# Kernel optimization log

Measured on AMD Instinct MI355X. Metric: run time of the kernel, lower is better.

The kernel has to match this reference:

```python
import jax, jax.numpy as jnp
import numpy as np

NUM_TOKENS = 8192
TWO_D = 22016  # 2 * intermediate_size (LLaMA-7B: d = 11008)
DEQUANT_SCALE = 0.0008


def setup_inputs() -> dict:
    key = jax.random.key(0)
    # int32 accumulators from an int8 gate_up GEMM: symmetric around 0
    x = jax.random.randint(key, (NUM_TOKENS, TWO_D), -128, 128, dtype=jnp.int32)
    dequant_scale = jnp.float32(DEQUANT_SCALE)
    return {"x": x, "dequant_scale": dequant_scale}


def reference(x, dequant_scale):
    # Dequant -> SiLU(gate) * up -> per-token abs-max int8 requant.
    d = x.shape[1] // 2
    xf = x.astype(jnp.float32) * dequant_scale          # dequantize
    gate = xf[:, :d]
    up = xf[:, d:]
    tmp = jax.nn.silu(gate) * up                        # (num_tokens, d) fp32
    # per-token quant scale = absmax / 127
    scale = jnp.max(jnp.abs(tmp), axis=1) / jnp.float32(127.0)  # (num_tokens,)
    q = jnp.clip(jnp.round(tmp / scale[:, None]), -128.0, 127.0).astype(jnp.int8)
    return (q, scale)
```

## Files before the change

### kernel.cpp

```cpp
#include <hip/hip_runtime.h>


constexpr int NUM_TOKENS = 8192;
constexpr int TWO_D      = 22016;
constexpr int D          = TWO_D / 2;
constexpr int VEC        = D / 4;
constexpr int THREADS    = 512;
constexpr int NWAVES     = THREADS / 64;
constexpr int FULL_ITERS = VEC / THREADS;
constexpr int REM        = VEC % THREADS;

typedef int   i32x4 __attribute__((ext_vector_type(4)));
typedef float f32x4 __attribute__((ext_vector_type(4)));

__device__ __forceinline__ float silu_mul(float g, float u) {
    return g * __builtin_amdgcn_rcpf(1.0f + __expf(-g)) * u;
}

__global__ __launch_bounds__(THREADS)
void dsmq_kernel(const i32x4* __restrict__ x,
                 const float* __restrict__ dsp,
                 f32x4* __restrict__ qout,
                 float* __restrict__ sout)
{
    const int row = blockIdx.x;
    const int t   = threadIdx.x;
    const float ds = *dsp;

    const i32x4* gp = x + (size_t)row * (TWO_D / 4);
    const i32x4* up = gp + VEC;

    f32x4 tmp[FULL_ITERS + 1];
    float m = 0.0f;

#pragma unroll
    for (int k = 0; k <= FULL_ITERS; ++k) {
        const int idx = k * THREADS + t;
        if (k < FULL_ITERS || t < REM) {
            const i32x4 gv = __builtin_nontemporal_load(&gp[idx]);
            const i32x4 uv = __builtin_nontemporal_load(&up[idx]);
            f32x4 r;
            r.x = silu_mul((float)gv.x * ds, (float)uv.x * ds);
            r.y = silu_mul((float)gv.y * ds, (float)uv.y * ds);
            r.z = silu_mul((float)gv.z * ds, (float)uv.z * ds);
            r.w = silu_mul((float)gv.w * ds, (float)uv.w * ds);
            tmp[k] = r;
            m = fmaxf(m, fmaxf(fmaxf(fabsf(r.x), fabsf(r.y)),
                               fmaxf(fabsf(r.z), fabsf(r.w))));
        }
    }

#pragma unroll
    for (int off = 32; off >= 1; off >>= 1)
        m = fmaxf(m, __shfl_xor(m, off, 64));

    __shared__ float smax[NWAVES];
    const int wave = t >> 6;
    if ((t & 63) == 0) smax[wave] = m;
    __syncthreads();
    m = smax[0];
#pragma unroll
    for (int w = 1; w < NWAVES; ++w) m = fmaxf(m, smax[w]);

    const float scale = m / 127.0f;
    const float inv   = (m > 0.0f) ? 127.0f / m : 0.0f;

    if (t == 0) sout[row] = scale;

    f32x4* qp = qout + (size_t)row * VEC;
#pragma unroll
    for (int k = 0; k <= FULL_ITERS; ++k) {
        const int idx = k * THREADS + t;
        if (k < FULL_ITERS || t < REM) {
            const f32x4 r = tmp[k];
            f32x4 q;
            q.x = fminf(fmaxf(rintf(r.x * inv), -128.0f), 127.0f);
            q.y = fminf(fmaxf(rintf(r.y * inv), -128.0f), 127.0f);
            q.z = fminf(fmaxf(rintf(r.z * inv), -128.0f), 127.0f);
            q.w = fminf(fmaxf(rintf(r.w * inv), -128.0f), 127.0f);
            __builtin_nontemporal_store(q, &qp[idx]);
        }
    }
}

extern "C" void kernel_launch(void* const* d_in, const int* in_sizes, int n_in,
                              void* d_out, int out_size, void* d_ws, size_t ws_size,
                              hipStream_t stream)
{
    const i32x4* x  = (const i32x4*)d_in[0];
    const float* ds = (const float*)d_in[1];
    f32x4* qout = (f32x4*)d_out;
    float* sout = (float*)d_out + (size_t)NUM_TOKENS * D;
    dsmq_kernel<<<NUM_TOKENS, THREADS, 0, stream>>>(x, ds, qout, sout);
}
```

Baseline: 181.0 us.

## Process two rows per block, overlapping row1 loads with row0 quantized stores

Each block now handles two tokens. The second row's loads and SiLU compute are interleaved with the quantize-and-store pass of the first row, so memory reads and writes overlap within a block instead of running in separate phases. The grid is halved, which cuts per-block launch and reduction overhead but gives fewer blocks to schedule. Register pressure stays similar because the tmp array is reused across the two rows.

```diff
diff --git a/kernel.cpp b/kernel.cpp
--- a/kernel.cpp
+++ b/kernel.cpp
@@ -7,6 +7,7 @@
 constexpr int VEC        = D / 4;
 constexpr int THREADS    = 512;
 constexpr int NWAVES     = THREADS / 64;
+constexpr int ITERS      = (VEC + THREADS - 1) / THREADS;
 constexpr int FULL_ITERS = VEC / THREADS;
 constexpr int REM        = VEC % THREADS;
 
@@ -17,68 +18,95 @@
     return g * __builtin_amdgcn_rcpf(1.0f + __expf(-g)) * u;
 }
 
+__device__ __forceinline__ f32x4 silu4(const i32x4 gv, const i32x4 uv, float ds, float& m) {
+    f32x4 r;
+    r.x = silu_mul((float)gv.x * ds, (float)uv.x * ds);
+    r.y = silu_mul((float)gv.y * ds, (float)uv.y * ds);
+    r.z = silu_mul((float)gv.z * ds, (float)uv.z * ds);
+    r.w = silu_mul((float)gv.w * ds, (float)uv.w * ds);
+    m = fmaxf(m, fmaxf(fmaxf(fabsf(r.x), fabsf(r.y)),
+                       fmaxf(fabsf(r.z), fabsf(r.w))));
+    return r;
+}
+
+__device__ __forceinline__ f32x4 quant4(const f32x4 r, float inv) {
+    f32x4 q;
+    q.x = fminf(fmaxf(rintf(r.x * inv), -128.0f), 127.0f);
+    q.y = fminf(fmaxf(rintf(r.y * inv), -128.0f), 127.0f);
+    q.z = fminf(fmaxf(rintf(r.z * inv), -128.0f), 127.0f);
+    q.w = fminf(fmaxf(rintf(r.w * inv), -128.0f), 127.0f);
+    return q;
+}
+
+__device__ __forceinline__ float block_max(float m, volatile float* smax, int t) {
+#pragma unroll
+    for (int off = 32; off >= 1; off >>= 1)
+        m = fmaxf(m, __shfl_xor(m, off, 64));
+    if ((t & 63) == 0) smax[t >> 6] = m;
+    __syncthreads();
+    float r = smax[0];
+#pragma unroll
+    for (int w = 1; w < NWAVES; ++w) r = fmaxf(r, smax[w]);
+    return r;
+}
+
 __global__ __launch_bounds__(THREADS)
 void dsmq_kernel(const i32x4* __restrict__ x,
                  const float* __restrict__ dsp,
                  f32x4* __restrict__ qout,
                  float* __restrict__ sout)
 {
-    const int row = blockIdx.x;
-    const int t   = threadIdx.x;
+    const int row0 = blockIdx.x * 2;
+    const int row1 = row0 + 1;
+    const int t    = threadIdx.x;
     const float ds = *dsp;
 
-    const i32x4* gp = x + (size_t)row * (TWO_D / 4);
-    const i32x4* up = gp + VEC;
+    const i32x4* g0 = x + (size_t)row0 * (TWO_D / 4);
+    const i32x4* u0 = g0 + VEC;
+    const i32x4* g1 = x + (size_t)row1 * (TWO_D / 4);
+    const i32x4* u1 = g1 + VEC;
+    f32x4* q0 = qout + (size_t)row0 * VEC;
+    f32x4* q1 = qout + (size_t)row1 * VEC;
 
-    f32x4 tmp[FULL_ITERS + 1];
-    float m = 0.0f;
+    __shared__ float smax0[NWAVES];
+    __shared__ float smax1[NWAVES];
+
+    f32x4 tmp[ITERS];
+    float m0 = 0.0f;
 
 #pragma unroll
-    for (int k = 0; k <= FULL_ITERS; ++k) {
+    for (int k = 0; k < ITERS; ++k) {
         const int idx = k * THREADS + t;
         if (k < FULL_ITERS || t < REM) {
-            const i32x4 gv = __builtin_nontemporal_load(&gp[idx]);
-            const i32x4 uv = __builtin_nontemporal_load(&up[idx]);
-            f32x4 r;
-            r.x = silu_mul((float)gv.x * ds, (float)uv.x * ds);
-            r.y = silu_mul((float)gv.y * ds, (float)uv.y * ds);
-            r.z = silu_mul((float)gv.z * ds, (float)uv.z * ds);
-            r.w = silu_mul((float)gv.w * ds, (float)uv.w * ds);
-            tmp[k] = r;
-            m = fmaxf(m, fmaxf(fmaxf(fabsf(r.x), fabsf(r.y)),
-                               fmaxf(fabsf(r.z), fabsf(r.w))));
+            const i32x4 gv = __builtin_nontemporal_load(&g0[idx]);
+            const i32x4 uv = __builtin_nontemporal_load(&u0[idx]);
+            tmp[k] = silu4(gv, uv, ds, m0);
         }
     }
+    m0 = block_max(m0, smax0, t);
+    const float inv0 = (m0 > 0.0f) ? 127.0f / m0 : 0.0f;
+    if (t == 0) sout[row0] = m0 / 127.0f;
+
+    float m1 = 0.0f;
+#pragma unroll
+    for (int k = 0; k < ITERS; ++k) {
+        const int idx = k * THREADS + t;
+        if (k < FULL_ITERS || t < REM) {
+            const i32x4 gv = __builtin_nontemporal_load(&g1[idx]);
+            const i32x4 uv = __builtin_nontemporal_load(&u1[idx]);
+            __builtin_nontemporal_store(quant4(tmp[k], inv0), &q0[idx]);
+            tmp[k] = silu4(gv, uv, ds, m1);
+        }
+    }
+    m1 = block_max(m1, smax1, t);
+    const float inv1 = (m1 > 0.0f) ? 127.0f / m1 : 0.0f;
+    if (t == 0) sout[row1] = m1 / 127.0f;
 
 #pragma unroll
-    for (int off = 32; off >= 1; off >>= 1)
-        m = fmaxf(m, __shfl_xor(m, off, 64));
-
-    __shared__ float smax[NWAVES];
-    const int wave = t >> 6;
-    if ((t & 63) == 0) smax[wave] = m;
-    __syncthreads();
-    m = smax[0];
-#pragma unroll
-    for (int w = 1; w < NWAVES; ++w) m = fmaxf(m, smax[w]);
-
-    const float scale = m / 127.0f;
-    const float inv   = (m > 0.0f) ? 127.0f / m : 0.0f;
-
-    if (t == 0) sout[row] = scale;
-
-    f32x4* qp = qout + (size_t)row * VEC;
-#pragma unroll
-    for (int k = 0; k <= FULL_ITERS; ++k) {
+    for (int k = 0; k < ITERS; ++k) {
         const int idx = k * THREADS + t;
         if (k < FULL_ITERS || t < REM) {
-            const f32x4 r = tmp[k];
-            f32x4 q;
-            q.x = fminf(fmaxf(rintf(r.x * inv), -128.0f), 127.0f);
-            q.y = fminf(fmaxf(rintf(r.y * inv), -128.0f), 127.0f);
-            q.z = fminf(fmaxf(rintf(r.z * inv), -128.0f), 127.0f);
-            q.w = fminf(fmaxf(rintf(r.w * inv), -128.0f), 127.0f);
-            __builtin_nontemporal_store(q, &qp[idx]);
+            __builtin_nontemporal_store(quant4(tmp[k], inv1), &q1[idx]);
         }
     }
 }
@@ -91,5 +119,5 @@
     const float* ds = (const float*)d_in[1];
     f32x4* qout = (f32x4*)d_out;
     float* sout = (float*)d_out + (size_t)NUM_TOKENS * D;
-    dsmq_kernel<<<NUM_TOKENS, THREADS, 0, stream>>>(x, ds, qout, sout);
+    dsmq_kernel<<<NUM_TOKENS / 2, THREADS, 0, stream>>>(x, ds, qout, sout);
 }
```

After: 191.0 us. 5.6% more time.
